# Performance work log

Measured on AMD Instinct MI355X. Metric: run time of the kernel, lower is better.

The kernel has to match this reference:

```python
import jax, jax.numpy as jnp
import numpy as np

H = 16
D_MODEL = 1024
D_K = D_MODEL // H


def setup_inputs() -> dict:
    key = jax.random.key(0)
    ks = jax.random.split(key, 12)
    B, S = 2, 2048
    scale = 1.0 / np.sqrt(D_MODEL)
    inp = {
        "query": jax.random.normal(ks[0], (B, S, D_MODEL), jnp.float32),
        "key": jax.random.normal(ks[1], (B, S, D_MODEL), jnp.float32),
        "value": jax.random.normal(ks[2], (B, S, D_MODEL), jnp.float32),
        "mask": jnp.ones((B, 1, S), jnp.int32),
        "Wq": jax.random.normal(ks[3], (D_MODEL, D_MODEL), jnp.float32) * scale,
        "bq": jnp.zeros((D_MODEL,), jnp.float32),
        "Wk": jax.random.normal(ks[4], (D_MODEL, D_MODEL), jnp.float32) * scale,
        "bk": jnp.zeros((D_MODEL,), jnp.float32),
        "Wv": jax.random.normal(ks[5], (D_MODEL, D_MODEL), jnp.float32) * scale,
        "bv": jnp.zeros((D_MODEL,), jnp.float32),
        "Wo": jax.random.normal(ks[6], (D_MODEL, D_MODEL), jnp.float32) * scale,
        "bo": jnp.zeros((D_MODEL,), jnp.float32),
    }
    return inp


def reference(query, key, value, mask, Wq, bq, Wk, bk, Wv, bv, Wo, bo):
    B, S, _ = query.shape
    # QKV projections, split heads: [B, S, D] -> [B, H, S, d_k]
    def proj(x, W, b):
        y = x @ W.T + b
        return y.reshape(B, -1, H, D_K).transpose(0, 2, 1, 3)

    q = proj(query, Wq, bq)
    k = proj(key, Wk, bk)
    v = proj(value, Wv, bv)

    # scaled dot-product attention with full score matrix [B, H, Sq, Sk]
    scores = jnp.einsum("bhqd,bhkd->bhqk", q, k) / np.sqrt(D_K)
    m = mask[:, None, :, :]  # unsqueeze head dim: [B, 1, 1_or_S, S]
    scores = jnp.where(m == 0, jnp.float32(-1e9), scores)
    p_attn = jax.nn.softmax(scores, axis=-1)  # dropout p=0.0 (eval)
    x = jnp.einsum("bhqk,bhkd->bhqd", p_attn, v)

    # merge heads and output projection
    x = x.transpose(0, 2, 1, 3).reshape(B, -1, H * D_K)
    return x @ Wo.T + bo
```

## Files before the change

### kernel.cpp

```cpp
#include <hip/hip_runtime.h>
#include <hip/hip_bf16.h>
#include <stdint.h>

typedef unsigned short us;
typedef __bf16 bf8 __attribute__((ext_vector_type(8)));
typedef float  f4  __attribute__((ext_vector_type(4)));

typedef unsigned int __attribute__((address_space(1))) as1_uint;
typedef unsigned int __attribute__((address_space(3))) as3_uint;

__device__ __forceinline__ void async_ld16(const void* g, void* l) {
    __builtin_amdgcn_global_load_lds((as1_uint*)g, (as3_uint*)l, 16, 0, 0);
}

__device__ __forceinline__ us f2bf(float f) {
    __hip_bfloat16 h = __float2bfloat16(f);
    us u;
    __builtin_memcpy(&u, &h, 2);
    return u;
}

__device__ __forceinline__ float fexp2(float x) {
#if __has_builtin(__builtin_amdgcn_exp2f)
    return __builtin_amdgcn_exp2f(x);
#else
    return exp2f(x);
#endif
}

#define SCALE_Q 0.18033688011112042f

__global__ __launch_bounds__(256)
void convert_all(const float* __restrict__ s0, const float* __restrict__ s1,
                 const float* __restrict__ s2, const float* __restrict__ s3,
                 const float* __restrict__ s4, const float* __restrict__ s5,
                 const float* __restrict__ s6,
                 us* __restrict__ d0, us* __restrict__ d1, us* __restrict__ d2,
                 us* __restrict__ d3, us* __restrict__ d4, us* __restrict__ d5,
                 us* __restrict__ d6)
{
    size_t i4 = (((size_t)blockIdx.x * 256) + threadIdx.x) << 2;
    const float* src; us* dst; size_t off;
    if (i4 < ((size_t)3 << 22)) {
        unsigned seg = (unsigned)(i4 >> 22);
        off = i4 & (((size_t)1 << 22) - 1);
        src = seg == 0 ? s0 : (seg == 1 ? s1 : s2);
        dst = seg == 0 ? d0 : (seg == 1 ? d1 : d2);
    } else {
        size_t j = i4 - ((size_t)3 << 22);
        unsigned seg = (unsigned)(j >> 20);
        off = j & (((size_t)1 << 20) - 1);
        src = seg == 0 ? s3 : (seg == 1 ? s4 : (seg == 2 ? s5 : s6));
        dst = seg == 0 ? d3 : (seg == 1 ? d4 : (seg == 2 ? d5 : d6));
    }
    float4 f = *(const float4*)(src + off);
    ushort4 o;
    o.x = f2bf(f.x); o.y = f2bf(f.y); o.z = f2bf(f.z); o.w = f2bf(f.w);
    *(ushort4*)(dst + off) = o;
}

template<int MODE, int BN>
__device__ __forceinline__
void gemm_body(const us* __restrict__ A, const us* __restrict__ W,
               const float* __restrict__ bias, void* __restrict__ out,
               float scale, int bx, int by)
{
    __shared__ us lA[128 * 32];
    __shared__ us lB[BN * 32];

    const int tid  = threadIdx.x;
    const int wv   = tid >> 6;
    const int lane = tid & 63;
    const int l15  = lane & 15;
    const int quad = lane >> 4;
    const int kq   = quad << 3;
    const int cr   = quad << 2;
    const int srow = lane >> 2;
    const int scol = (lane & 3) << 3;
    const int m0   = by << 7;
    const int n0   = bx * BN;
    constexpr int MJ = (BN == 128) ? 4 : 2;
    const int wm = (BN == 128) ? ((wv >> 1) << 6) : (wv << 5);
    const int wn = (BN == 128) ? ((wv & 1) << 6) : 0;

    f4 acc[4][MJ];
    const f4 zero = {0.f, 0.f, 0.f, 0.f};
#pragma unroll
    for (int i = 0; i < 4; ++i)
#pragma unroll
        for (int j = 0; j < MJ; ++j) acc[i][j] = zero;

    for (int kt = 0; kt < 1024; kt += 32) {
#pragma unroll
        for (int s = 0; s < 2; ++s) {
            const int chunk = wv * 2 + s;
            const int row   = chunk * 16 + srow;
            async_ld16(A + (size_t)(m0 + row) * 1024 + kt + scol, &lA[chunk * 512]);
        }
        if (BN == 128) {
#pragma unroll
            for (int s = 0; s < 2; ++s) {
                const int chunk = wv * 2 + s;
                const int row   = chunk * 16 + srow;
                async_ld16(W + (size_t)(n0 + row) * 1024 + kt + scol, &lB[chunk * 512]);
            }
        } else {
            const int row = wv * 16 + srow;
            async_ld16(W + (size_t)(n0 + row) * 1024 + kt + scol, &lB[wv * 512]);
        }
        __syncthreads();

        bf8 wf[4], xf[MJ];
#pragma unroll
        for (int i = 0; i < 4; ++i)
            wf[i] = *(const bf8*)&lB[(wn + i * 16 + l15) * 32 + kq];
#pragma unroll
        for (int j = 0; j < MJ; ++j)
            xf[j] = *(const bf8*)&lA[(wm + j * 16 + l15) * 32 + kq];
#pragma unroll
        for (int i = 0; i < 4; ++i)
#pragma unroll
            for (int j = 0; j < MJ; ++j)
                acc[i][j] = __builtin_amdgcn_mfma_f32_16x16x32_bf16(wf[i], xf[j], acc[i][j], 0, 0, 0);
        __syncthreads();
    }

    if (MODE == 2) {
        us* o = (us*)out;
#pragma unroll
        for (int j = 0; j < MJ; ++j) {
            const int f = m0 + wm + j * 16 + l15;
            const float bf_ = bias[f];
            const int hh = f >> 6, dd = f & 63;
#pragma unroll
            for (int i = 0; i < 4; ++i) {
                const int tokb = n0 + wn + i * 16 + cr;
                const int bb = tokb >> 11, ss = tokb & 2047;
                us hp[4];
#pragma unroll
                for (int r = 0; r < 4; ++r) hp[r] = f2bf(acc[i][j][r] + bf_);
                uint2 w;
                w.x = (unsigned)hp[0] | ((unsigned)hp[1] << 16);
                w.y = (unsigned)hp[2] | ((unsigned)hp[3] << 16);
                *(uint2*)&o[((size_t)((bb * 16 + hh) * 64 + dd) << 11) + ss] = w;
            }
        }
        return;
    }

#pragma unroll
    for (int i = 0; i < 4; ++i) {
        const int gnb = n0 + wn + i * 16 + cr;
        const f4 bj = *(const f4*)&bias[gnb];
        if (MODE == 0) {
            us* o = (us*)out;
            const int hh = gnb >> 6, dd = gnb & 63;
#pragma unroll
            for (int j = 0; j < MJ; ++j) {
                const int gm = m0 + wm + j * 16 + l15;
                const int bb = gm >> 11, ss = gm & 2047;
                us hp[4];
#pragma unroll
                for (int r = 0; r < 4; ++r)
                    hp[r] = f2bf((acc[i][j][r] + bj[r]) * scale);
                uint2 w;
                w.x = (unsigned)hp[0] | ((unsigned)hp[1] << 16);
                w.y = (unsigned)hp[2] | ((unsigned)hp[3] << 16);
                *(uint2*)&o[(((size_t)(bb * 16 + hh) * 2048 + ss) << 6) + dd] = w;
            }
        } else {
            float* o = (float*)out;
#pragma unroll
            for (int j = 0; j < MJ; ++j) {
                const int gm = m0 + wm + j * 16 + l15;
                f4 v;
#pragma unroll
                for (int r = 0; r < 4; ++r) v[r] = acc[i][j][r] + bj[r];
                *(f4*)&o[((size_t)gm << 10) + gnb] = v;
            }
        }
    }
}

__global__ __launch_bounds__(256)
void gemm_qkv(const us* __restrict__ XQ, const us* __restrict__ XK,
              const us* __restrict__ XV,
              const us* __restrict__ WQ, const us* __restrict__ WK,
              const us* __restrict__ WV,
              const float* __restrict__ bq, const float* __restrict__ bk,
              const float* __restrict__ bv,
              us* __restrict__ QP, us* __restrict__ KP, us* __restrict__ VT)
{
    const int z = blockIdx.z;
    if (z == 2) {
        gemm_body<2, 128>(WV, XV, bv, VT, 1.0f, blockIdx.y, blockIdx.x);
        return;
    }
    const us* A = z == 0 ? XQ : XK;
    const us* W = z == 0 ? WQ : WK;
    const float* b = z == 0 ? bq : bk;
    us* o = z == 0 ? QP : KP;
    const float scale = z == 0 ? SCALE_Q : 1.0f;
    gemm_body<0, 128>(A, W, b, o, scale, blockIdx.x, blockIdx.y);
}

__global__ __launch_bounds__(256)
void gemm_o(const us* __restrict__ A, const us* __restrict__ W,
            const float* __restrict__ bias, float* __restrict__ out)
{
    gemm_body<1, 64>(A, W, bias, out, 1.0f, blockIdx.x, blockIdx.y);
}

__global__ __launch_bounds__(256)
void flash_attn(const us* __restrict__ Qp, const us* __restrict__ Kp,
                const us* __restrict__ Vtp, const int* __restrict__ maskp,
                us* __restrict__ ctx)
{
    __shared__ us lK[2][64 * 64];
    __shared__ us lVt[2][64 * 64];
    __shared__ us lP[4 * 32 * 72];
    __shared__ float lmask[2][64];

    const int tid  = threadIdx.x;
    const int wv   = tid >> 6;
    const int lane = tid & 63;
    const int l15  = lane & 15;
    const int quad = lane >> 4;
    const int cr   = quad << 2;
    const int l7   = l15 & 7;

    const int q0 = blockIdx.x << 7;
    const int h  = blockIdx.y;
    const int b  = blockIdx.z;

    const size_t headoff = ((size_t)(b * 16 + h)) << 17;
    const us* Qh  = Qp  + headoff;
    const us* Kh  = Kp  + headoff;
    const us* Vth = Vtp + headoff;

    bf8 qf[2][2];
#pragma unroll
    for (int nt = 0; nt < 2; ++nt)
#pragma unroll
        for (int kb = 0; kb < 2; ++kb)
            qf[nt][kb] = *(const bf8*)(Qh + ((size_t)(q0 + wv * 32 + nt * 16 + l15) << 6)
                                          + kb * 32 + (quad << 3));

    const f4 zero = {0.f, 0.f, 0.f, 0.f};
    f4 of[4][2];
#pragma unroll
    for (int dt = 0; dt < 4; ++dt)
#pragma unroll
        for (int nt = 0; nt < 2; ++nt) of[dt][nt] = zero;
    float li[2] = {0.f, 0.f};

    us* lPw = lP + wv * (32 * 72);

    const int sr = tid >> 3;
    const int sc = tid & 7;

    uint4 rk[2], rv[2];
    float rm = 1.0f;

#define FA_ISSUE(kt0)                                                          \
    {                                                                          \
        _Pragma("unroll")                                                      \
        for (int it = 0; it < 2; ++it) {                                       \
            const int r = sr + 32 * it;                                        \
            rk[it] = *(const uint4*)(Kh + ((size_t)((kt0) + r) << 6) + sc * 8);\
            rv[it] = *(const uint4*)(Vth + (size_t)r * 2048 + (kt0) + sc * 8); \
        }                                                                      \
        if (tid < 64)                                                          \
            rm = (maskp[((size_t)b << 11) + (kt0) + tid] == 0) ? 0.0f : 1.0f;  \
    }

#define FA_WRITE(bi)                                                           \
    {                                                                          \
        _Pragma("unroll")                                                      \
        for (int it = 0; it < 2; ++it) {                                       \
            const int r = sr + 32 * it;                                        \
            const int sw = (sc ^ (r & 7)) << 3;                                \
            *(uint4*)&lK[bi][(r << 6) + sw] = rk[it];                          \
            *(uint4*)&lVt[bi][(r << 6) + sw] = rv[it];                         \
        }                                                                      \
        if (tid < 64) lmask[bi][tid] = rm;                                     \
    }

    FA_ISSUE(0);
    FA_WRITE(0);
    FA_ISSUE(64);
    __syncthreads();

    for (int t = 0; t < 32; ++t) {
        const int cur = t & 1;
        const us* lKc  = lK[cur];
        const us* lVtc = lVt[cur];

        float rs[2] = {0.f, 0.f};
#pragma unroll
        for (int kt = 0; kt < 4; ++kt) {
            const int krow = (kt * 16 + l15) << 6;
            bf8 kf0 = *(const bf8*)&lKc[krow + ((quad ^ l7) << 3)];
            bf8 kf1 = *(const bf8*)&lKc[krow + (((4 + quad) ^ l7) << 3)];
            f4 st[2];
#pragma unroll
            for (int nt = 0; nt < 2; ++nt) {
                st[nt] = __builtin_amdgcn_mfma_f32_16x16x32_bf16(kf0, qf[nt][0], zero, 0, 0, 0);
                st[nt] = __builtin_amdgcn_mfma_f32_16x16x32_bf16(kf1, qf[nt][1], st[nt], 0, 0, 0);
            }
            const f4 mr = *(const f4*)&lmask[cur][kt * 16 + cr];
#pragma unroll
            for (int nt = 0; nt < 2; ++nt) {
                us hp[4];
#pragma unroll
                for (int r = 0; r < 4; ++r) {
                    const float p = fexp2(st[nt][r]) * mr[r];
                    rs[nt] += p;
                    hp[r] = f2bf(p);
                }
                uint2 w;
                w.x = (unsigned)hp[0] | ((unsigned)hp[1] << 16);
                w.y = (unsigned)hp[2] | ((unsigned)hp[3] << 16);
                *(uint2*)&lPw[(nt * 16 + l15) * 72 + kt * 16 + cr] = w;
            }
        }
#pragma unroll
        for (int nt = 0; nt < 2; ++nt) {
            float r2 = rs[nt];
            r2 += __shfl_xor(r2, 16, 64);
            r2 += __shfl_xor(r2, 32, 64);
            li[nt] += r2;
        }

#pragma unroll
        for (int kb = 0; kb < 2; ++kb) {
            bf8 pfr[2];
#pragma unroll
            for (int nt = 0; nt < 2; ++nt)
                pfr[nt] = *(const bf8*)&lPw[(nt * 16 + l15) * 72 + kb * 32 + (quad << 3)];
#pragma unroll
            for (int dt = 0; dt < 4; ++dt) {
                bf8 vf = *(const bf8*)&lVtc[((dt * 16 + l15) << 6) + (((kb * 4 + quad) ^ l7) << 3)];
#pragma unroll
                for (int nt = 0; nt < 2; ++nt)
                    of[dt][nt] = __builtin_amdgcn_mfma_f32_16x16x32_bf16(vf, pfr[nt], of[dt][nt], 0, 0, 0);
            }
        }

        if (t < 31) {
            __syncthreads();
            FA_WRITE(cur ^ 1);
            if (t < 30) FA_ISSUE((t + 2) * 64);
            __syncthreads();
        }
    }
#undef FA_ISSUE
#undef FA_WRITE

#pragma unroll
    for (int nt = 0; nt < 2; ++nt) {
        const float linv = 1.0f / li[nt];
        const int tok = q0 + wv * 32 + nt * 16 + l15;
        const size_t rowb = (((size_t)(b * 2048 + tok)) << 10) + (h << 6);
#pragma unroll
        for (int dt = 0; dt < 4; ++dt) {
            us hp[4];
#pragma unroll
            for (int r = 0; r < 4; ++r) hp[r] = f2bf(of[dt][nt][r] * linv);
            uint2 w;
            w.x = (unsigned)hp[0] | ((unsigned)hp[1] << 16);
            w.y = (unsigned)hp[2] | ((unsigned)hp[3] << 16);
            *(uint2*)&ctx[rowb + dt * 16 + cr] = w;
        }
    }
}

extern "C" void kernel_launch(void* const* d_in, const int* in_sizes, int n_in,
                              void* d_out, int out_size, void* d_ws, size_t ws_size,
                              hipStream_t stream)
{
    const float* q    = (const float*)d_in[0];
    const float* k    = (const float*)d_in[1];
    const float* v    = (const float*)d_in[2];
    const int*   mask = (const int*)d_in[3];
    const float* Wq   = (const float*)d_in[4];
    const float* bq   = (const float*)d_in[5];
    const float* Wk   = (const float*)d_in[6];
    const float* bk   = (const float*)d_in[7];
    const float* Wv   = (const float*)d_in[8];
    const float* bv   = (const float*)d_in[9];
    const float* Wo   = (const float*)d_in[10];
    const float* bo   = (const float*)d_in[11];
    float* out = (float*)d_out;

    us* ws  = (us*)d_ws;
    us* XQ  = ws;
    us* XK  = ws + 4194304;
    us* XV  = ws + 8388608;
    us* WQb = ws + 12582912;
    us* WKb = ws + 13631488;
    us* WVb = ws + 14680064;
    us* WOb = ws + 15728640;
    us* QP  = ws + 16777216;
    us* KP  = ws + 20971520;
    us* VT  = ws + 25165824;
    us* CTX = XQ;

    convert_all<<<16384, 256, 0, stream>>>(q, k, v, Wq, Wk, Wv, Wo,
                                           XQ, XK, XV, WQb, WKb, WVb, WOb);
    gemm_qkv<<<dim3(8, 32, 3), 256, 0, stream>>>(XQ, XK, XV, WQb, WKb, WVb,
                                                 bq, bk, bv, QP, KP, VT);
    flash_attn<<<dim3(16, 16, 2), 256, 0, stream>>>(QP, KP, VT, mask, CTX);
    gemm_o<<<dim3(16, 32), 256, 0, stream>>>(CTX, WOb, bo, out);
}
```

Before: 278.1 us.

## Stream K/V tiles into LDS with async global_load_lds and one barrier per step

Register-staged K/V prefetch is replaced with direct global-to-LDS asynchronous loads (global_load_lds). The swizzle is kept by permuting the source address per lane instead of the LDS destination. The loop now issues the next tile's loads into the other buffer right after a single barrier at the top of each iteration, which cuts the two barriers per step to one and frees the staging registers. In exchange, prefetch distance drops from two tiles ahead to one, and correctness depends on the barrier waiting for outstanding async LDS writes.

```diff
diff --git a/kernel.cpp b/kernel.cpp
--- a/kernel.cpp
+++ b/kernel.cpp
@@ -238,6 +238,9 @@
     const us* Kh  = Kp  + headoff;
     const us* Vth = Vtp + headoff;
 
+    const int gr    = lane >> 3;
+    const int gslot = ((lane & 7) ^ gr) << 3;
+
     bf8 qf[2][2];
 #pragma unroll
     for (int nt = 0; nt < 2; ++nt)
@@ -256,43 +259,29 @@
 
     us* lPw = lP + wv * (32 * 72);
 
-    const int sr = tid >> 3;
-    const int sc = tid & 7;
-
-    uint4 rk[2], rv[2];
-    float rm = 1.0f;
-
-#define FA_ISSUE(kt0)                                                          \
+#define FA_ISSUE(kt0, bi)                                                      \
     {                                                                          \
         _Pragma("unroll")                                                      \
-        for (int it = 0; it < 2; ++it) {                                       \
-            const int r = sr + 32 * it;                                        \
-            rk[it] = *(const uint4*)(Kh + ((size_t)((kt0) + r) << 6) + sc * 8);\
-            rv[it] = *(const uint4*)(Vth + (size_t)r * 2048 + (kt0) + sc * 8); \
+        for (int i = 0; i < 2; ++i) {                                          \
+            const int rbase = wv * 16 + i * 8;                                 \
+            const int r = rbase + gr;                                          \
+            async_ld16(Kh + ((size_t)((kt0) + r) << 6) + gslot,                \
+                       &lK[bi][rbase * 64]);                                   \
+            async_ld16(Vth + (size_t)r * 2048 + (kt0) + gslot,                 \
+                       &lVt[bi][rbase * 64]);                                  \
         }                                                                      \
         if (tid < 64)                                                          \
-            rm = (maskp[((size_t)b << 11) + (kt0) + tid] == 0) ? 0.0f : 1.0f;  \
-    }
-
-#define FA_WRITE(bi)                                                           \
-    {                                                                          \
-        _Pragma("unroll")                                                      \
-        for (int it = 0; it < 2; ++it) {                                       \
-            const int r = sr + 32 * it;                                        \
-            const int sw = (sc ^ (r & 7)) << 3;                                \
-            *(uint4*)&lK[bi][(r << 6) + sw] = rk[it];                          \
-            *(uint4*)&lVt[bi][(r << 6) + sw] = rv[it];                         \
-        }                                                                      \
-        if (tid < 64) lmask[bi][tid] = rm;                                     \
-    }
-
-    FA_ISSUE(0);
-    FA_WRITE(0);
-    FA_ISSUE(64);
-    __syncthreads();
+            lmask[bi][tid] =                                                   \
+                (maskp[((size_t)b << 11) + (kt0) + tid] == 0) ? 0.0f : 1.0f;   \
+    }
+
+    FA_ISSUE(0, 0);
 
     for (int t = 0; t < 32; ++t) {
         const int cur = t & 1;
+        __syncthreads();
+        if (t < 31) FA_ISSUE((t + 1) * 64, cur ^ 1);
+
         const us* lKc  = lK[cur];
         const us* lVtc = lVt[cur];
 
@@ -346,16 +335,8 @@
                     of[dt][nt] = __builtin_amdgcn_mfma_f32_16x16x32_bf16(vf, pfr[nt], of[dt][nt], 0, 0, 0);
             }
         }
-
-        if (t < 31) {
-            __syncthreads();
-            FA_WRITE(cur ^ 1);
-            if (t < 30) FA_ISSUE((t + 2) * 64);
-            __syncthreads();
-        }
     }
 #undef FA_ISSUE
-#undef FA_WRITE
 
 #pragma unroll
     for (int nt = 0; nt < 2; ++nt) {
```

Measured after the change: 248.2 us. -10.7%, faster.
